# Performance work log

Measured on AMD Instinct MI355X. Metric: run time of the kernel, lower is better.

The kernel has to match this reference:

```python
import math
import jax, jax.numpy as jnp
import numpy as np

NUM_FREQ = 10  # NeRF-style L=10 -> enc dim 3 + 3*2*10 = 63

def pos_encode(coords):
    # freq_bands = 2^i * pi, i = 0..L-1
    freq = (2.0 ** jnp.arange(NUM_FREQ, dtype=coords.dtype)) * math.pi
    scaled = coords[..., None] * freq                      # [E, 3, L]
    enc = jnp.stack([jnp.sin(scaled), jnp.cos(scaled)], axis=-1)  # [E, 3, L, 2]
    enc = enc.reshape(coords.shape[0], -1)                 # [E, 60] interleaved sin/cos
    return jnp.concatenate([coords, enc], axis=-1)         # [E, 63]

def setup_inputs() -> dict:
    key = jax.random.key(0)
    ks = jax.random.split(key, 9)
    N, M, K, C = 65536, 16384, 32, 64
    E = M * K
    x = jax.random.normal(ks[0], (N, C), jnp.float32)
    pos = jax.random.normal(ks[1], (N, 3), jnp.float32)
    batch = jnp.sort(jax.random.randint(ks[2], (N,), 0, 8))
    idx = jax.random.randint(ks[3], (M,), 0, N)
    row = jnp.sort(jax.random.randint(ks[4], (E,), 0, M))
    col = jax.random.randint(ks[5], (E,), 0, N)
    d_in = C + 3 + 3 * 2 * NUM_FREQ  # 127
    def lin(k, i, o):
        s = 1.0 / np.sqrt(i)
        kw, kb = jax.random.split(k)
        return (jax.random.uniform(kw, (i, o), jnp.float32, -s, s),
                jax.random.uniform(kb, (o,), jnp.float32, -s, s))
    lw1, lb1 = lin(ks[6], d_in, 128)
    lw2, lb2 = lin(ks[7], 128, 128)
    gw, gb = lin(ks[8], 128, 256)
    return dict(x=x, pos=pos, batch=batch, idx=idx, row=row, col=col,
                lw1=lw1, lb1=lb1, lw2=lw2, lb2=lb2, gw=gw, gb=gb)

def reference(x, pos, batch, idx, row, col, lw1, lb1, lw2, lb2, gw, gb):
    M = idx.shape[0]
    pos_idx = pos[idx]                         # [M, 3] sampled centers
    pos_diff = pos[col] - pos_idx[row]         # [E, 3] neighbor offsets
    pe = pos_encode(pos_diff)                  # [E, 63]
    edge_in = jnp.concatenate([x[col], pe], axis=-1)   # [E, 127]
    # local_nn: Linear->ReLU->Linear (no final activation, per MLP_Wrapper)
    h = jax.nn.relu(edge_in @ lw1 + lb1)       # [E, 128]
    edge_feat = h @ lw2 + lb2                  # [E, 128]
    # scatter_reduce amax, include_self=False: empty rows stay 0
    agg = jax.ops.segment_max(edge_feat, row, num_segments=M)
    agg = jnp.where(jnp.isneginf(agg), jnp.zeros((), agg.dtype), agg)
    out = agg @ gw + gb                        # [M, 256] global_nn (single Linear)
    return out, pos_idx, batch[idx]
```

## Files before the change

kernel.cpp:

```cpp
#include <hip/hip_runtime.h>
#include <math.h>

#define NN 65536
#define MM 16384
#define EE 524288
#define CF 64
#define HD 128
#define OD 256
#define RPB 16
#define PITCH 129

typedef __bf16 bf16x8 __attribute__((ext_vector_type(8)));
typedef __bf16 bf16x4 __attribute__((ext_vector_type(4)));
typedef float f32x4 __attribute__((ext_vector_type(4)));

__device__ __forceinline__ unsigned enc_f(float f) {
    unsigned u = __float_as_uint(f);
    return (u & 0x80000000u) ? ~u : (u | 0x80000000u);
}
__device__ __forceinline__ float dec_f(unsigned e) {
    unsigned u = (e & 0x80000000u) ? (e ^ 0x80000000u) : ~e;
    return __uint_as_float(u);
}
#define ENC_NEG_INF 0x007FFFFFu

__device__ __forceinline__ unsigned bf_bits(float f) {
    __bf16 b = (__bf16)f;
    return (unsigned)__builtin_bit_cast(unsigned short, b);
}

#define WS_FRAG_OFF 0
#define WS_ROWPTR_OFF 65536
#define WS_XBF_OFF 131072
#define WS_PD_OFF (131072 + 8388608)

__global__ void k_pre(__bf16* __restrict__ fragbuf, int* __restrict__ rowptr,
                      __bf16* __restrict__ xbf, float4* __restrict__ pdbuf,
                      const float* __restrict__ lw1, const float* __restrict__ lw2,
                      const float* __restrict__ x, const int* __restrict__ row,
                      const int* __restrict__ col,
                      const float* __restrict__ pos, const int* __restrict__ batch,
                      const int* __restrict__ idx, float* __restrict__ out) {
    const int b = blockIdx.x;
    const int t = threadIdx.x;
    if (b == 0) {
        const int lane = t & 63;
        const int wv = t >> 6;
        const int q = lane >> 4;
        const int ln = lane & 15;
        #pragma unroll
        for (int fi = 0; fi < 16; ++fi) {
            const int nt = (fi >> 2) & 1, kk = fi & 3;
            const int n = wv * 32 + nt * 16 + ln;
            bf16x8 f;
            #pragma unroll
            for (int j = 0; j < 8; ++j) {
                const int c = kk * 32 + q * 8 + j;
                const int rk = (c < 67) ? c : c - 1;
                f[j] = (fi < 8) ? (__bf16)((c == 67) ? 0.0f : lw1[rk * HD + n])
                                : (__bf16)lw2[c * HD + n];
            }
            *(bf16x8*)&fragbuf[((size_t)fi * 256 + t) * 8] = f;
        }
    } else if (b <= 65) {
        const int i = (b - 1) * 256 + t;
        if (i <= MM) {
            int lo = 0, hi = EE;
            while (lo < hi) { int mid = (lo + hi) >> 1; if (row[mid] < i) lo = mid + 1; else hi = mid; }
            rowptr[i] = lo;
        }
    } else if (b <= 129) {
        const int m = (b - 66) * 256 + t;
        if (m < MM) {
            const int s = idx[m];
            out[MM * OD + m * 3 + 0] = pos[s * 3 + 0];
            out[MM * OD + m * 3 + 1] = pos[s * 3 + 1];
            out[MM * OD + m * 3 + 2] = pos[s * 3 + 2];
            out[MM * OD + MM * 3 + m] = (float)batch[s];
        }
    } else if (b <= 1153) {
        const size_t base = ((size_t)(b - 130) * 256 + t) * 16;
        const float4* xs = (const float4*)(x + base);
        const float4 a = xs[0], c = xs[1], d = xs[2], e = xs[3];
        bf16x8 o0, o1;
        o0[0] = (__bf16)a.x; o0[1] = (__bf16)a.y; o0[2] = (__bf16)a.z; o0[3] = (__bf16)a.w;
        o0[4] = (__bf16)c.x; o0[5] = (__bf16)c.y; o0[6] = (__bf16)c.z; o0[7] = (__bf16)c.w;
        o1[0] = (__bf16)d.x; o1[1] = (__bf16)d.y; o1[2] = (__bf16)d.z; o1[3] = (__bf16)d.w;
        o1[4] = (__bf16)e.x; o1[5] = (__bf16)e.y; o1[6] = (__bf16)e.z; o1[7] = (__bf16)e.w;
        *(bf16x8*)&xbf[base] = o0;
        *(bf16x8*)&xbf[base + 8] = o1;
    } else {
        const int e = (b - 1154) * 256 + t;
        const int r = row[e];
        const int c = col[e];
        const int s = idx[r];
        float4 pd;
        pd.x = pos[c * 3 + 0] - pos[s * 3 + 0];
        pd.y = pos[c * 3 + 1] - pos[s * 3 + 1];
        pd.z = pos[c * 3 + 2] - pos[s * 3 + 2];
        pd.w = 0.0f;
        pdbuf[e] = pd;
    }
}

__launch_bounds__(256)
__global__ void k_fused(const __bf16* __restrict__ xbf, const float4* __restrict__ pdbuf,
                        const int* __restrict__ row, const int* __restrict__ col,
                        const int* __restrict__ rowptr, const __bf16* __restrict__ fragbuf,
                        const float* __restrict__ lb1, const float* __restrict__ lb2,
                        const float* __restrict__ gw, const float* __restrict__ gb,
                        float* __restrict__ out) {
    __shared__ __align__(16) __bf16 einX[64][64];
    __shared__ __align__(16) __bf16 einP[64][64];
    __shared__ __align__(16) __bf16 hbuf[64][HD];
    __shared__ unsigned maxbuf[(RPB + 1) * PITCH];
    __shared__ int srow[2][64];
    const int t = threadIdx.x;
    const int lane = t & 63;
    const int wv = t >> 6;
    const int q = lane >> 4;
    const int ln = lane & 15;
    const int lsw = ln & 7;
    const int m0 = blockIdx.x * RPB;

    const int es = rowptr[m0];
    const int ee = rowptr[m0 + RPB];
    const int ntiles = (ee - es + 63) >> 6;

    for (int i = t; i < (RPB + 1) * PITCH; i += 256) maxbuf[i] = ENC_NEG_INF;

    const int pe_e = t >> 2, pe_part = t & 3, pe_esw = pe_e & 7;
    bf16x8 s0, s1;
    auto issue = [&](int tt) {
        const int eg = min(es + tt * 64 + pe_e, EE - 1);
        const int c = col[eg];
        const bf16x8* xr = (const bf16x8*)(xbf + (size_t)c * CF) + pe_part * 2;
        s0 = xr[0]; s1 = xr[1];
    };
    auto commit = [&]() {
        *(bf16x8*)&einX[pe_e][((pe_part * 2 + 0) ^ pe_esw) * 8] = s0;
        *(bf16x8*)&einX[pe_e][((pe_part * 2 + 1) ^ pe_esw) * 8] = s1;
    };
    auto do_pe = [&](int tt) {
        if (t < 192) {
            const int e = t & 63, d = t >> 6;
            const int sb = tt & 1;
            const int eidx = es + tt * 64 + e;
            const int eg = min(eidx, EE - 1);
            const int esw = e & 7;
            const float4 P = pdbuf[eg];
            const float pd = (d == 0) ? P.x : ((d == 1) ? P.y : P.z);
            if (d == 0) {
                srow[sb][e] = (eidx < ee) ? (row[eg] - m0) : RPB;
                uint2 pkt;
                pkt.x = bf_bits(P.x) | (bf_bits(P.y) << 16);
                pkt.y = bf_bits(P.z);
                *(uint2*)&einP[e][esw * 8] = pkt;
            }
            const float fr = __builtin_amdgcn_fractf(pd * 0.5f);
            float sv = __builtin_amdgcn_sinf(fr);
            float cv = __builtin_amdgcn_cosf(fr);
            #pragma unroll
            for (int l = 0; l < 10; ++l) {
                const int jP = 4 + d * 20 + l * 2;
                *(unsigned*)&einP[e][((jP >> 3) ^ esw) * 8 + (jP & 7)] =
                    bf_bits(sv) | (bf_bits(cv) << 16);
                const float s2 = 2.0f * sv * cv;
                const float c2 = 1.0f - 2.0f * sv * sv;
                sv = s2; cv = c2;
            }
        }
    };

    bf16x8 w1f[2][4];
    #pragma unroll
    for (int nt = 0; nt < 2; ++nt)
        #pragma unroll
        for (int kk = 0; kk < 4; ++kk)
            w1f[nt][kk] = *(const bf16x8*)&fragbuf[((size_t)(nt * 4 + kk) * 256 + t) * 8];
    float4 b1q[2];
    #pragma unroll
    for (int nt = 0; nt < 2; ++nt)
        b1q[nt] = *(const float4*)&lb1[wv * 32 + nt * 16 + q * 4];

    if (ntiles > 0) {
        issue(0);
        commit();
        do_pe(0);
        if (ntiles > 1) issue(1);
    }
    __syncthreads();

    for (int tt = 0; tt < ntiles; ++tt) {
        f32x4 acc[2][4];
        #pragma unroll
        for (int nt = 0; nt < 2; ++nt)
            #pragma unroll
            for (int et = 0; et < 4; ++et)
                acc[nt][et] = (f32x4){b1q[nt].x, b1q[nt].y, b1q[nt].z, b1q[nt].w};
        #pragma unroll
        for (int et = 0; et < 4; ++et) {
            const int e = et * 16 + ln;
            bf16x8 a[4];
            a[0] = *(const bf16x8*)&einX[e][(q ^ lsw) * 8];
            a[1] = *(const bf16x8*)&einX[e][((4 + q) ^ lsw) * 8];
            a[2] = *(const bf16x8*)&einP[e][(q ^ lsw) * 8];
            a[3] = *(const bf16x8*)&einP[e][((4 + q) ^ lsw) * 8];
            #pragma unroll
            for (int kk = 0; kk < 4; ++kk) {
                acc[0][et] = __builtin_amdgcn_mfma_f32_16x16x32_bf16(w1f[0][kk], a[kk], acc[0][et], 0, 0, 0);
                acc[1][et] = __builtin_amdgcn_mfma_f32_16x16x32_bf16(w1f[1][kk], a[kk], acc[1][et], 0, 0, 0);
            }
        }
        #pragma unroll
        for (int et = 0; et < 4; ++et) {
            const int e = et * 16 + ln;
            #pragma unroll
            for (int nt = 0; nt < 2; ++nt) {
                bf16x4 hv;
                hv[0] = (__bf16)fmaxf(acc[nt][et][0], 0.0f);
                hv[1] = (__bf16)fmaxf(acc[nt][et][1], 0.0f);
                hv[2] = (__bf16)fmaxf(acc[nt][et][2], 0.0f);
                hv[3] = (__bf16)fmaxf(acc[nt][et][3], 0.0f);
                const int chunk = wv * 4 + nt * 2 + (q >> 1);
                *(bf16x4*)&hbuf[e][((chunk ^ lsw) * 8) + (q & 1) * 4] = hv;
            }
        }
        __syncthreads();

        {
            if (tt + 1 < ntiles) { commit(); issue(tt + 2 < ntiles ? tt + 2 : tt + 1); }
            bf16x8 w2f[2][4];
            #pragma unroll
            for (int nt = 0; nt < 2; ++nt)
                #pragma unroll
                for (int kk = 0; kk < 4; ++kk)
                    w2f[nt][kk] = *(const bf16x8*)&fragbuf[((size_t)(8 + nt * 4 + kk) * 256 + t) * 8];

            f32x4 acc2[4][2];
            #pragma unroll
            for (int nt = 0; nt < 2; ++nt) {
                const float b2 = lb2[wv * 32 + nt * 16 + ln];
                #pragma unroll
                for (int et = 0; et < 4; ++et)
                    acc2[et][nt] = (f32x4){b2, b2, b2, b2};
            }
            #pragma unroll
            for (int et = 0; et < 4; ++et) {
                const int e = et * 16 + ln;
                #pragma unroll
                for (int kk = 0; kk < 4; ++kk) {
                    bf16x8 ah = *(const bf16x8*)&hbuf[e][((kk * 4 + q) ^ lsw) * 8];
                    acc2[et][0] = __builtin_amdgcn_mfma_f32_16x16x32_bf16(ah, w2f[0][kk], acc2[et][0], 0, 0, 0);
                    acc2[et][1] = __builtin_amdgcn_mfma_f32_16x16x32_bf16(ah, w2f[1][kk], acc2[et][1], 0, 0, 0);
                }
            }
            if (tt + 1 < ntiles) do_pe(tt + 1);
            const int sb = tt & 1;
            #pragma unroll
            for (int et = 0; et < 4; ++et) {
                const int4 R = *(const int4*)&srow[sb][et * 16 + q * 4];
                #pragma unroll
                for (int nt = 0; nt < 2; ++nt) {
                    unsigned* base = maxbuf + (wv * 32 + nt * 16 + ln);
                    const f32x4 vv = acc2[et][nt];
                    int cur = R.x;
                    float m = vv[0];
                    if (R.y != cur) { atomicMax(base + cur * PITCH, enc_f(m)); cur = R.y; m = vv[1]; }
                    else m = fmaxf(m, vv[1]);
                    if (R.z != cur) { atomicMax(base + cur * PITCH, enc_f(m)); cur = R.z; m = vv[2]; }
                    else m = fmaxf(m, vv[2]);
                    if (R.w != cur) { atomicMax(base + cur * PITCH, enc_f(m)); cur = R.w; m = vv[3]; }
                    else m = fmaxf(m, vv[3]);
                    atomicMax(base + cur * PITCH, enc_f(m));
                }
            }
        }
        __syncthreads();
    }

    float* afin = (float*)hbuf;
    for (int i = t; i < RPB * HD; i += 256) {
        const unsigned e = maxbuf[(i >> 7) * PITCH + (i & 127)];
        afin[i] = (e == ENC_NEG_INF) ? 0.0f : dec_f(e);
    }
    __syncthreads();

    const int j4 = (t & 63) * 4;
    const int rbase = (t >> 6) * 4;
    float facc[4][4];
    const float4 bias = *(const float4*)&gb[j4];
    #pragma unroll
    for (int r = 0; r < 4; ++r) { facc[r][0] = bias.x; facc[r][1] = bias.y; facc[r][2] = bias.z; facc[r][3] = bias.w; }
    for (int k = 0; k < 128; k += 4) {
        float4 w0 = *(const float4*)&gw[(k + 0) * OD + j4];
        float4 w1 = *(const float4*)&gw[(k + 1) * OD + j4];
        float4 w2 = *(const float4*)&gw[(k + 2) * OD + j4];
        float4 w3 = *(const float4*)&gw[(k + 3) * OD + j4];
        #pragma unroll
        for (int r = 0; r < 4; ++r) {
            float4 av = *(const float4*)&afin[(rbase + r) * HD + k];
            facc[r][0] += av.x * w0.x + av.y * w1.x + av.z * w2.x + av.w * w3.x;
            facc[r][1] += av.x * w0.y + av.y * w1.y + av.z * w2.y + av.w * w3.y;
            facc[r][2] += av.x * w0.z + av.y * w1.z + av.z * w2.z + av.w * w3.z;
            facc[r][3] += av.x * w0.w + av.y * w1.w + av.z * w2.w + av.w * w3.w;
        }
    }
    #pragma unroll
    for (int r = 0; r < 4; ++r) {
        float4 v; v.x = facc[r][0]; v.y = facc[r][1]; v.z = facc[r][2]; v.w = facc[r][3];
        *(float4*)&out[(size_t)(m0 + rbase + r) * OD + j4] = v;
    }
}

extern "C" void kernel_launch(void* const* d_in, const int* in_sizes, int n_in,
                              void* d_out, int out_size, void* d_ws, size_t ws_size,
                              hipStream_t stream) {
    const float* x   = (const float*)d_in[0];
    const float* pos = (const float*)d_in[1];
    const int* batch = (const int*)d_in[2];
    const int* idx   = (const int*)d_in[3];
    const int* row   = (const int*)d_in[4];
    const int* col   = (const int*)d_in[5];
    const float* lw1 = (const float*)d_in[6];
    const float* lb1 = (const float*)d_in[7];
    const float* lw2 = (const float*)d_in[8];
    const float* lb2 = (const float*)d_in[9];
    const float* gw  = (const float*)d_in[10];
    const float* gb  = (const float*)d_in[11];
    float* out = (float*)d_out;
    __bf16* fragbuf = (__bf16*)((char*)d_ws + WS_FRAG_OFF);
    int* rowptr     = (int*)((char*)d_ws + WS_ROWPTR_OFF);
    __bf16* xbf     = (__bf16*)((char*)d_ws + WS_XBF_OFF);
    float4* pdbuf   = (float4*)((char*)d_ws + WS_PD_OFF);

    hipLaunchKernelGGL(k_pre, dim3(1 + 65 + 64 + 1024 + 2048), dim3(256), 0, stream,
                       fragbuf, rowptr, xbf, pdbuf, lw1, lw2, x, row, col, pos, batch, idx, out);
    hipLaunchKernelGGL(k_fused, dim3(MM / RPB), dim3(256), 0, stream,
                       xbf, pdbuf, row, col, rowptr, fragbuf, lb1, lb2, gw, gb, out);
}
```

Measured before the change: 99.77 us.

## Use 512-thread blocks with each wave owning one 16-column MFMA tile

Doubles the fused kernel's block size to 8 waves so each wave computes a single 16-wide output column slice of both MLP layers instead of two. The weight fragment layout, the gather of x rows (one 16-byte load per thread), the max-scatter and the final global linear are all re-partitioned across 512 threads. This lowers per-thread register pressure and raises the number of waves available to hide gather latency, at the cost of more threads contending for the same barriers and LDS atomics.

```diff
diff --git a/kernel.cpp b/kernel.cpp
--- a/kernel.cpp
+++ b/kernel.cpp
@@ -9,6 +9,7 @@
 #define OD 256
 #define RPB 16
 #define PITCH 129
+#define BT 512
 
 typedef __bf16 bf16x8 __attribute__((ext_vector_type(8)));
 typedef __bf16 bf16x4 __attribute__((ext_vector_type(4)));
@@ -44,23 +45,24 @@
     const int b = blockIdx.x;
     const int t = threadIdx.x;
     if (b == 0) {
-        const int lane = t & 63;
-        const int wv = t >> 6;
-        const int q = lane >> 4;
-        const int ln = lane & 15;
-        #pragma unroll
-        for (int fi = 0; fi < 16; ++fi) {
-            const int nt = (fi >> 2) & 1, kk = fi & 3;
-            const int n = wv * 32 + nt * 16 + ln;
-            bf16x8 f;
-            #pragma unroll
-            for (int j = 0; j < 8; ++j) {
-                const int c = kk * 32 + q * 8 + j;
-                const int rk = (c < 67) ? c : c - 1;
-                f[j] = (fi < 8) ? (__bf16)((c == 67) ? 0.0f : lw1[rk * HD + n])
-                                : (__bf16)lw2[c * HD + n];
-            }
-            *(bf16x8*)&fragbuf[((size_t)fi * 256 + t) * 8] = f;
+        for (int tt = t; tt < BT; tt += 256) {
+            const int lane = tt & 63;
+            const int q = (lane >> 4);
+            const int ln = lane & 15;
+            const int n = (tt >> 6) * 16 + ln;
+            #pragma unroll
+            for (int fi = 0; fi < 8; ++fi) {
+                const int kk = fi & 3;
+                bf16x8 f;
+                #pragma unroll
+                for (int j = 0; j < 8; ++j) {
+                    const int c = kk * 32 + q * 8 + j;
+                    const int rk = (c < 67) ? c : c - 1;
+                    f[j] = (fi < 4) ? (__bf16)((c == 67) ? 0.0f : lw1[rk * HD + n])
+                                    : (__bf16)lw2[c * HD + n];
+                }
+                *(bf16x8*)&fragbuf[((size_t)fi * BT + tt) * 8] = f;
+            }
         }
     } else if (b <= 65) {
         const int i = (b - 1) * 256 + t;
@@ -103,7 +105,7 @@
     }
 }
 
-__launch_bounds__(256)
+__launch_bounds__(BT)
 __global__ void k_fused(const __bf16* __restrict__ xbf, const float4* __restrict__ pdbuf,
                         const int* __restrict__ row, const int* __restrict__ col,
                         const int* __restrict__ rowptr, const __bf16* __restrict__ fragbuf,
@@ -121,25 +123,24 @@
     const int q = lane >> 4;
     const int ln = lane & 15;
     const int lsw = ln & 7;
+    const int n0 = wv * 16;
     const int m0 = blockIdx.x * RPB;
 
     const int es = rowptr[m0];
     const int ee = rowptr[m0 + RPB];
     const int ntiles = (ee - es + 63) >> 6;
 
-    for (int i = t; i < (RPB + 1) * PITCH; i += 256) maxbuf[i] = ENC_NEG_INF;
-
-    const int pe_e = t >> 2, pe_part = t & 3, pe_esw = pe_e & 7;
-    bf16x8 s0, s1;
+    for (int i = t; i < (RPB + 1) * PITCH; i += BT) maxbuf[i] = ENC_NEG_INF;
+
+    const int pe_e = t >> 3, pe_part = t & 7, pe_esw = pe_e & 7;
+    bf16x8 s0;
     auto issue = [&](int tt) {
         const int eg = min(es + tt * 64 + pe_e, EE - 1);
         const int c = col[eg];
-        const bf16x8* xr = (const bf16x8*)(xbf + (size_t)c * CF) + pe_part * 2;
-        s0 = xr[0]; s1 = xr[1];
+        s0 = *(const bf16x8*)(xbf + (size_t)c * CF + pe_part * 8);
     };
     auto commit = [&]() {
-        *(bf16x8*)&einX[pe_e][((pe_part * 2 + 0) ^ pe_esw) * 8] = s0;
-        *(bf16x8*)&einX[pe_e][((pe_part * 2 + 1) ^ pe_esw) * 8] = s1;
+        *(bf16x8*)&einX[pe_e][(pe_part ^ pe_esw) * 8] = s0;
     };
     auto do_pe = [&](int tt) {
         if (t < 192) {
@@ -172,16 +173,11 @@
         }
     };
 
-    bf16x8 w1f[2][4];
+    bf16x8 w1f[4];
     #pragma unroll
-    for (int nt = 0; nt < 2; ++nt)
-        #pragma unroll
-        for (int kk = 0; kk < 4; ++kk)
-            w1f[nt][kk] = *(const bf16x8*)&fragbuf[((size_t)(nt * 4 + kk) * 256 + t) * 8];
-    float4 b1q[2];
-    #pragma unroll
-    for (int nt = 0; nt < 2; ++nt)
-        b1q[nt] = *(const float4*)&lb1[wv * 32 + nt * 16 + q * 4];
+    for (int kk = 0; kk < 4; ++kk)
+        w1f[kk] = *(const bf16x8*)&fragbuf[((size_t)kk * BT + t) * 8];
+    const float4 b1q = *(const float4*)&lb1[n0 + q * 4];
 
     if (ntiles > 0) {
         issue(0);
@@ -192,12 +188,10 @@
     __syncthreads();
 
     for (int tt = 0; tt < ntiles; ++tt) {
-        f32x4 acc[2][4];
+        f32x4 acc[4];
         #pragma unroll
-        for (int nt = 0; nt < 2; ++nt)
-            #pragma unroll
-            for (int et = 0; et < 4; ++et)
-                acc[nt][et] = (f32x4){b1q[nt].x, b1q[nt].y, b1q[nt].z, b1q[nt].w};
+        for (int et = 0; et < 4; ++et)
+            acc[et] = (f32x4){b1q.x, b1q.y, b1q.z, b1q.w};
         #pragma unroll
         for (int et = 0; et < 4; ++et) {
             const int e = et * 16 + ln;
@@ -207,52 +201,41 @@
             a[2] = *(const bf16x8*)&einP[e][(q ^ lsw) * 8];
             a[3] = *(const bf16x8*)&einP[e][((4 + q) ^ lsw) * 8];
             #pragma unroll
-            for (int kk = 0; kk < 4; ++kk) {
-                acc[0][et] = __builtin_amdgcn_mfma_f32_16x16x32_bf16(w1f[0][kk], a[kk], acc[0][et], 0, 0, 0);
-                acc[1][et] = __builtin_amdgcn_mfma_f32_16x16x32_bf16(w1f[1][kk], a[kk], acc[1][et], 0, 0, 0);
-            }
+            for (int kk = 0; kk < 4; ++kk)
+                acc[et] = __builtin_amdgcn_mfma_f32_16x16x32_bf16(w1f[kk], a[kk], acc[et], 0, 0, 0);
         }
         #pragma unroll
         for (int et = 0; et < 4; ++et) {
             const int e = et * 16 + ln;
-            #pragma unroll
-            for (int nt = 0; nt < 2; ++nt) {
-                bf16x4 hv;
-                hv[0] = (__bf16)fmaxf(acc[nt][et][0], 0.0f);
-                hv[1] = (__bf16)fmaxf(acc[nt][et][1], 0.0f);
-                hv[2] = (__bf16)fmaxf(acc[nt][et][2], 0.0f);
-                hv[3] = (__bf16)fmaxf(acc[nt][et][3], 0.0f);
-                const int chunk = wv * 4 + nt * 2 + (q >> 1);
-                *(bf16x4*)&hbuf[e][((chunk ^ lsw) * 8) + (q & 1) * 4] = hv;
-            }
+            bf16x4 hv;
+            hv[0] = (__bf16)fmaxf(acc[et][0], 0.0f);
+            hv[1] = (__bf16)fmaxf(acc[et][1], 0.0f);
+            hv[2] = (__bf16)fmaxf(acc[et][2], 0.0f);
+            hv[3] = (__bf16)fmaxf(acc[et][3], 0.0f);
+            const int chunk = wv * 2 + (q >> 1);
+            *(bf16x4*)&hbuf[e][((chunk ^ lsw) * 8) + (q & 1) * 4] = hv;
         }
         __syncthreads();
 
         {
             if (tt + 1 < ntiles) { commit(); issue(tt + 2 < ntiles ? tt + 2 : tt + 1); }
-            bf16x8 w2f[2][4];
-            #pragma unroll
-            for (int nt = 0; nt < 2; ++nt)
-                #pragma unroll
-                for (int kk = 0; kk < 4; ++kk)
-                    w2f[nt][kk] = *(const bf16x8*)&fragbuf[((size_t)(8 + nt * 4 + kk) * 256 + t) * 8];
-
-            f32x4 acc2[4][2];
-            #pragma unroll
-            for (int nt = 0; nt < 2; ++nt) {
-                const float b2 = lb2[wv * 32 + nt * 16 + ln];
-                #pragma unroll
-                for (int et = 0; et < 4; ++et)
-                    acc2[et][nt] = (f32x4){b2, b2, b2, b2};
-            }
+            bf16x8 w2f[4];
+            #pragma unroll
+            for (int kk = 0; kk < 4; ++kk)
+                w2f[kk] = *(const bf16x8*)&fragbuf[((size_t)(4 + kk) * BT + t) * 8];
+
+            const float b2 = lb2[n0 + ln];
+            f32x4 acc2[4];
+            #pragma unroll
+            for (int et = 0; et < 4; ++et)
+                acc2[et] = (f32x4){b2, b2, b2, b2};
             #pragma unroll
             for (int et = 0; et < 4; ++et) {
                 const int e = et * 16 + ln;
                 #pragma unroll
                 for (int kk = 0; kk < 4; ++kk) {
                     bf16x8 ah = *(const bf16x8*)&hbuf[e][((kk * 4 + q) ^ lsw) * 8];
-                    acc2[et][0] = __builtin_amdgcn_mfma_f32_16x16x32_bf16(ah, w2f[0][kk], acc2[et][0], 0, 0, 0);
-                    acc2[et][1] = __builtin_amdgcn_mfma_f32_16x16x32_bf16(ah, w2f[1][kk], acc2[et][1], 0, 0, 0);
+                    acc2[et] = __builtin_amdgcn_mfma_f32_16x16x32_bf16(ah, w2f[kk], acc2[et], 0, 0, 0);
                 }
             }
             if (tt + 1 < ntiles) do_pe(tt + 1);
@@ -260,45 +243,42 @@
             #pragma unroll
             for (int et = 0; et < 4; ++et) {
                 const int4 R = *(const int4*)&srow[sb][et * 16 + q * 4];
-                #pragma unroll
-                for (int nt = 0; nt < 2; ++nt) {
-                    unsigned* base = maxbuf + (wv * 32 + nt * 16 + ln);
-                    const f32x4 vv = acc2[et][nt];
-                    int cur = R.x;
-                    float m = vv[0];
-                    if (R.y != cur) { atomicMax(base + cur * PITCH, enc_f(m)); cur = R.y; m = vv[1]; }
-                    else m = fmaxf(m, vv[1]);
-                    if (R.z != cur) { atomicMax(base + cur * PITCH, enc_f(m)); cur = R.z; m = vv[2]; }
-                    else m = fmaxf(m, vv[2]);
-                    if (R.w != cur) { atomicMax(base + cur * PITCH, enc_f(m)); cur = R.w; m = vv[3]; }
-                    else m = fmaxf(m, vv[3]);
-                    atomicMax(base + cur * PITCH, enc_f(m));
-                }
+                unsigned* base = maxbuf + (n0 + ln);
+                const f32x4 vv = acc2[et];
+                int cur = R.x;
+                float m = vv[0];
+                if (R.y != cur) { atomicMax(base + cur * PITCH, enc_f(m)); cur = R.y; m = vv[1]; }
+                else m = fmaxf(m, vv[1]);
+                if (R.z != cur) { atomicMax(base + cur * PITCH, enc_f(m)); cur = R.z; m = vv[2]; }
+                else m = fmaxf(m, vv[2]);
+                if (R.w != cur) { atomicMax(base + cur * PITCH, enc_f(m)); cur = R.w; m = vv[3]; }
+                else m = fmaxf(m, vv[3]);
+                atomicMax(base + cur * PITCH, enc_f(m));
             }
         }
         __syncthreads();
     }
 
     float* afin = (float*)hbuf;
-    for (int i = t; i < RPB * HD; i += 256) {
+    for (int i = t; i < RPB * HD; i += BT) {
         const unsigned e = maxbuf[(i >> 7) * PITCH + (i & 127)];
         afin[i] = (e == ENC_NEG_INF) ? 0.0f : dec_f(e);
     }
     __syncthreads();
 
     const int j4 = (t & 63) * 4;
-    const int rbase = (t >> 6) * 4;
-    float facc[4][4];
+    const int rbase = (t >> 6) * 2;
+    float facc[2][4];
     const float4 bias = *(const float4*)&gb[j4];
     #pragma unroll
-    for (int r = 0; r < 4; ++r) { facc[r][0] = bias.x; facc[r][1] = bias.y; facc[r][2] = bias.z; facc[r][3] = bias.w; }
+    for (int r = 0; r < 2; ++r) { facc[r][0] = bias.x; facc[r][1] = bias.y; facc[r][2] = bias.z; facc[r][3] = bias.w; }
     for (int k = 0; k < 128; k += 4) {
         float4 w0 = *(const float4*)&gw[(k + 0) * OD + j4];
         float4 w1 = *(const float4*)&gw[(k + 1) * OD + j4];
         float4 w2 = *(const float4*)&gw[(k + 2) * OD + j4];
         float4 w3 = *(const float4*)&gw[(k + 3) * OD + j4];
         #pragma unroll
-        for (int r = 0; r < 4; ++r) {
+        for (int r = 0; r < 2; ++r) {
             float4 av = *(const float4*)&afin[(rbase + r) * HD + k];
             facc[r][0] += av.x * w0.x + av.y * w1.x + av.z * w2.x + av.w * w3.x;
             facc[r][1] += av.x * w0.y + av.y * w1.y + av.z * w2.y + av.w * w3.y;
@@ -307,7 +287,7 @@
         }
     }
     #pragma unroll
-    for (int r = 0; r < 4; ++r) {
+    for (int r = 0; r < 2; ++r) {
         float4 v; v.x = facc[r][0]; v.y = facc[r][1]; v.z = facc[r][2]; v.w = facc[r][3];
         *(float4*)&out[(size_t)(m0 + rbase + r) * OD + j4] = v;
     }
@@ -336,6 +316,6 @@
 
     hipLaunchKernelGGL(k_pre, dim3(1 + 65 + 64 + 1024 + 2048), dim3(256), 0, stream,
                        fragbuf, rowptr, xbf, pdbuf, lw1, lw2, x, row, col, pos, batch, idx, out);
-    hipLaunchKernelGGL(k_fused, dim3(MM / RPB), dim3(256), 0, stream,
+    hipLaunchKernelGGL(k_fused, dim3(MM / RPB), dim3(BT), 0, stream,
                        xbf, pdbuf, row, col, rowptr, fragbuf, lb1, lb2, gw, gb, out);
 }
```

After: 104.4 us. 4.7% more time.

## Load gathered x rows directly into MFMA fragments, dropping LDS staging

Applied to the files above, without the earlier changes.

Removes the einX shared-memory buffer and the software-pipelined issue/commit prefetch of gathered x[col] rows. Each wave now loads its col indices and reads its bf16 x fragments straight from global memory into registers just before the first-layer MFMAs. This saves LDS space and LDS write/read traffic, which may help occupancy. The cost is that the gather latency is no longer hidden behind the previous tile's work, and the four waves each fetch the same rows redundantly.

```diff
diff --git a/kernel.cpp b/kernel.cpp
--- a/kernel.cpp
+++ b/kernel.cpp
@@ -110,7 +110,6 @@
                         const float* __restrict__ lb1, const float* __restrict__ lb2,
                         const float* __restrict__ gw, const float* __restrict__ gb,
                         float* __restrict__ out) {
-    __shared__ __align__(16) __bf16 einX[64][64];
     __shared__ __align__(16) __bf16 einP[64][64];
     __shared__ __align__(16) __bf16 hbuf[64][HD];
     __shared__ unsigned maxbuf[(RPB + 1) * PITCH];
@@ -129,18 +128,6 @@
 
     for (int i = t; i < (RPB + 1) * PITCH; i += 256) maxbuf[i] = ENC_NEG_INF;
 
-    const int pe_e = t >> 2, pe_part = t & 3, pe_esw = pe_e & 7;
-    bf16x8 s0, s1;
-    auto issue = [&](int tt) {
-        const int eg = min(es + tt * 64 + pe_e, EE - 1);
-        const int c = col[eg];
-        const bf16x8* xr = (const bf16x8*)(xbf + (size_t)c * CF) + pe_part * 2;
-        s0 = xr[0]; s1 = xr[1];
-    };
-    auto commit = [&]() {
-        *(bf16x8*)&einX[pe_e][((pe_part * 2 + 0) ^ pe_esw) * 8] = s0;
-        *(bf16x8*)&einX[pe_e][((pe_part * 2 + 1) ^ pe_esw) * 8] = s1;
-    };
     auto do_pe = [&](int tt) {
         if (t < 192) {
             const int e = t & 63, d = t >> 6;
@@ -183,15 +170,17 @@
     for (int nt = 0; nt < 2; ++nt)
         b1q[nt] = *(const float4*)&lb1[wv * 32 + nt * 16 + q * 4];
 
-    if (ntiles > 0) {
-        issue(0);
-        commit();
-        do_pe(0);
-        if (ntiles > 1) issue(1);
-    }
+    if (ntiles > 0) do_pe(0);
     __syncthreads();
 
     for (int tt = 0; tt < ntiles; ++tt) {
+        const int ebase = es + tt * 64;
+
+        int cvals[4];
+        #pragma unroll
+        for (int et = 0; et < 4; ++et)
+            cvals[et] = col[min(ebase + et * 16 + ln, EE - 1)];
+
         f32x4 acc[2][4];
         #pragma unroll
         for (int nt = 0; nt < 2; ++nt)
@@ -201,16 +190,19 @@
         #pragma unroll
         for (int et = 0; et < 4; ++et) {
             const int e = et * 16 + ln;
-            bf16x8 a[4];
-            a[0] = *(const bf16x8*)&einX[e][(q ^ lsw) * 8];
-            a[1] = *(const bf16x8*)&einX[e][((4 + q) ^ lsw) * 8];
-            a[2] = *(const bf16x8*)&einP[e][(q ^ lsw) * 8];
-            a[3] = *(const bf16x8*)&einP[e][((4 + q) ^ lsw) * 8];
-            #pragma unroll
-            for (int kk = 0; kk < 4; ++kk) {
-                acc[0][et] = __builtin_amdgcn_mfma_f32_16x16x32_bf16(w1f[0][kk], a[kk], acc[0][et], 0, 0, 0);
-                acc[1][et] = __builtin_amdgcn_mfma_f32_16x16x32_bf16(w1f[1][kk], a[kk], acc[1][et], 0, 0, 0);
-            }
+            const __bf16* xp = xbf + (size_t)cvals[et] * CF + q * 8;
+            bf16x8 a0 = *(const bf16x8*)xp;
+            bf16x8 a1 = *(const bf16x8*)(xp + 32);
+            bf16x8 a2 = *(const bf16x8*)&einP[e][(q ^ lsw) * 8];
+            bf16x8 a3 = *(const bf16x8*)&einP[e][((4 + q) ^ lsw) * 8];
+            acc[0][et] = __builtin_amdgcn_mfma_f32_16x16x32_bf16(w1f[0][0], a0, acc[0][et], 0, 0, 0);
+            acc[1][et] = __builtin_amdgcn_mfma_f32_16x16x32_bf16(w1f[1][0], a0, acc[1][et], 0, 0, 0);
+            acc[0][et] = __builtin_amdgcn_mfma_f32_16x16x32_bf16(w1f[0][1], a1, acc[0][et], 0, 0, 0);
+            acc[1][et] = __builtin_amdgcn_mfma_f32_16x16x32_bf16(w1f[1][1], a1, acc[1][et], 0, 0, 0);
+            acc[0][et] = __builtin_amdgcn_mfma_f32_16x16x32_bf16(w1f[0][2], a2, acc[0][et], 0, 0, 0);
+            acc[1][et] = __builtin_amdgcn_mfma_f32_16x16x32_bf16(w1f[1][2], a2, acc[1][et], 0, 0, 0);
+            acc[0][et] = __builtin_amdgcn_mfma_f32_16x16x32_bf16(w1f[0][3], a3, acc[0][et], 0, 0, 0);
+            acc[1][et] = __builtin_amdgcn_mfma_f32_16x16x32_bf16(w1f[1][3], a3, acc[1][et], 0, 0, 0);
         }
         #pragma unroll
         for (int et = 0; et < 4; ++et) {
@@ -229,7 +221,6 @@
         __syncthreads();
 
         {
-            if (tt + 1 < ntiles) { commit(); issue(tt + 2 < ntiles ? tt + 2 : tt + 1); }
             bf16x8 w2f[2][4];
             #pragma unroll
             for (int nt = 0; nt < 2; ++nt)
```

Result: slower. 121.7 us (+21.9%).

## Enlarge edge tile to 128 and restructure gather prefetch schedule

Applied to the files above, without the earlier changes.

Doubles the per-iteration edge tile from 64 to 128 edges, processing each tile as two 64-edge halves for both MLP layers. The goal is fewer barriers and loop iterations per block and more work between synchronisations. The x-feature gather prefetch now runs one tile ahead and is issued during the first layer-1 half instead of two tiles ahead. Shared memory use roughly doubles, which may lower occupancy, and the shorter prefetch distance could expose more gather latency.

```diff
diff --git a/kernel.cpp b/kernel.cpp
--- a/kernel.cpp
+++ b/kernel.cpp
@@ -8,6 +8,7 @@
 #define HD 128
 #define OD 256
 #define RPB 16
+#define ET 128
 #define PITCH 129
 
 typedef __bf16 bf16x8 __attribute__((ext_vector_type(8)));
@@ -110,11 +111,11 @@
                         const float* __restrict__ lb1, const float* __restrict__ lb2,
                         const float* __restrict__ gw, const float* __restrict__ gb,
                         float* __restrict__ out) {
-    __shared__ __align__(16) __bf16 einX[64][64];
-    __shared__ __align__(16) __bf16 einP[64][64];
-    __shared__ __align__(16) __bf16 hbuf[64][HD];
+    __shared__ __align__(16) __bf16 einX[ET][64];
+    __shared__ __align__(16) __bf16 einP[ET][64];
+    __shared__ __align__(16) __bf16 hbuf[ET][HD];
     __shared__ unsigned maxbuf[(RPB + 1) * PITCH];
-    __shared__ int srow[2][64];
+    __shared__ int srow[2][ET];
     const int t = threadIdx.x;
     const int lane = t & 63;
     const int wv = t >> 6;
@@ -125,49 +126,55 @@
 
     const int es = rowptr[m0];
     const int ee = rowptr[m0 + RPB];
-    const int ntiles = (ee - es + 63) >> 6;
+    const int ntiles = (ee - es + ET - 1) >> 7;
 
     for (int i = t; i < (RPB + 1) * PITCH; i += 256) maxbuf[i] = ENC_NEG_INF;
 
-    const int pe_e = t >> 2, pe_part = t & 3, pe_esw = pe_e & 7;
-    bf16x8 s0, s1;
+    const int pe_e = t >> 1, pe_part = t & 1, pe_esw = pe_e & 7;
+    bf16x8 s0, s1, s2, s3;
     auto issue = [&](int tt) {
-        const int eg = min(es + tt * 64 + pe_e, EE - 1);
+        const int eg = min(es + tt * ET + pe_e, EE - 1);
         const int c = col[eg];
-        const bf16x8* xr = (const bf16x8*)(xbf + (size_t)c * CF) + pe_part * 2;
-        s0 = xr[0]; s1 = xr[1];
+        const bf16x8* xr = (const bf16x8*)(xbf + (size_t)c * CF + pe_part * 32);
+        s0 = xr[0]; s1 = xr[1]; s2 = xr[2]; s3 = xr[3];
     };
     auto commit = [&]() {
-        *(bf16x8*)&einX[pe_e][((pe_part * 2 + 0) ^ pe_esw) * 8] = s0;
-        *(bf16x8*)&einX[pe_e][((pe_part * 2 + 1) ^ pe_esw) * 8] = s1;
+        *(bf16x8*)&einX[pe_e][((pe_part * 4 + 0) ^ pe_esw) * 8] = s0;
+        *(bf16x8*)&einX[pe_e][((pe_part * 4 + 1) ^ pe_esw) * 8] = s1;
+        *(bf16x8*)&einX[pe_e][((pe_part * 4 + 2) ^ pe_esw) * 8] = s2;
+        *(bf16x8*)&einX[pe_e][((pe_part * 4 + 3) ^ pe_esw) * 8] = s3;
     };
     auto do_pe = [&](int tt) {
-        if (t < 192) {
-            const int e = t & 63, d = t >> 6;
-            const int sb = tt & 1;
-            const int eidx = es + tt * 64 + e;
-            const int eg = min(eidx, EE - 1);
-            const int esw = e & 7;
-            const float4 P = pdbuf[eg];
-            const float pd = (d == 0) ? P.x : ((d == 1) ? P.y : P.z);
-            if (d == 0) {
-                srow[sb][e] = (eidx < ee) ? (row[eg] - m0) : RPB;
-                uint2 pkt;
-                pkt.x = bf_bits(P.x) | (bf_bits(P.y) << 16);
-                pkt.y = bf_bits(P.z);
-                *(uint2*)&einP[e][esw * 8] = pkt;
-            }
-            const float fr = __builtin_amdgcn_fractf(pd * 0.5f);
-            float sv = __builtin_amdgcn_sinf(fr);
-            float cv = __builtin_amdgcn_cosf(fr);
-            #pragma unroll
-            for (int l = 0; l < 10; ++l) {
-                const int jP = 4 + d * 20 + l * 2;
-                *(unsigned*)&einP[e][((jP >> 3) ^ esw) * 8 + (jP & 7)] =
-                    bf_bits(sv) | (bf_bits(cv) << 16);
-                const float s2 = 2.0f * sv * cv;
-                const float c2 = 1.0f - 2.0f * sv * sv;
-                sv = s2; cv = c2;
+        const int sb = tt & 1;
+        #pragma unroll
+        for (int i = 0; i < 2; ++i) {
+            const int p = i * 256 + t;
+            if (p < 384) {
+                const int e = p & 127, d = p >> 7;
+                const int eidx = es + tt * ET + e;
+                const int eg = min(eidx, EE - 1);
+                const int esw = e & 7;
+                const float4 P = pdbuf[eg];
+                const float pd = (d == 0) ? P.x : ((d == 1) ? P.y : P.z);
+                if (d == 0) {
+                    srow[sb][e] = (eidx < ee) ? (row[eg] - m0) : RPB;
+                    uint2 pkt;
+                    pkt.x = bf_bits(P.x) | (bf_bits(P.y) << 16);
+                    pkt.y = bf_bits(P.z);
+                    *(uint2*)&einP[e][esw * 8] = pkt;
+                }
+                const float fr = __builtin_amdgcn_fractf(pd * 0.5f);
+                float sv = __builtin_amdgcn_sinf(fr);
+                float cv = __builtin_amdgcn_cosf(fr);
+                #pragma unroll
+                for (int l = 0; l < 10; ++l) {
+                    const int jP = 4 + d * 20 + l * 2;
+                    *(unsigned*)&einP[e][((jP >> 3) ^ esw) * 8 + (jP & 7)] =
+                        bf_bits(sv) | (bf_bits(cv) << 16);
+                    const float s2 = 2.0f * sv * cv;
+                    const float c2 = 1.0f - 2.0f * sv * sv;
+                    sv = s2; cv = c2;
+                }
             }
         }
     };
@@ -192,88 +199,95 @@
     __syncthreads();
 
     for (int tt = 0; tt < ntiles; ++tt) {
-        f32x4 acc[2][4];
-        #pragma unroll
-        for (int nt = 0; nt < 2; ++nt)
-            #pragma unroll
-            for (int et = 0; et < 4; ++et)
-                acc[nt][et] = (f32x4){b1q[nt].x, b1q[nt].y, b1q[nt].z, b1q[nt].w};
-        #pragma unroll
-        for (int et = 0; et < 4; ++et) {
-            const int e = et * 16 + ln;
-            bf16x8 a[4];
-            a[0] = *(const bf16x8*)&einX[e][(q ^ lsw) * 8];
-            a[1] = *(const bf16x8*)&einX[e][((4 + q) ^ lsw) * 8];
-            a[2] = *(const bf16x8*)&einP[e][(q ^ lsw) * 8];
-            a[3] = *(const bf16x8*)&einP[e][((4 + q) ^ lsw) * 8];
-            #pragma unroll
-            for (int kk = 0; kk < 4; ++kk) {
-                acc[0][et] = __builtin_amdgcn_mfma_f32_16x16x32_bf16(w1f[0][kk], a[kk], acc[0][et], 0, 0, 0);
-                acc[1][et] = __builtin_amdgcn_mfma_f32_16x16x32_bf16(w1f[1][kk], a[kk], acc[1][et], 0, 0, 0);
-            }
-        }
-        #pragma unroll
-        for (int et = 0; et < 4; ++et) {
-            const int e = et * 16 + ln;
-            #pragma unroll
-            for (int nt = 0; nt < 2; ++nt) {
-                bf16x4 hv;
-                hv[0] = (__bf16)fmaxf(acc[nt][et][0], 0.0f);
-                hv[1] = (__bf16)fmaxf(acc[nt][et][1], 0.0f);
-                hv[2] = (__bf16)fmaxf(acc[nt][et][2], 0.0f);
-                hv[3] = (__bf16)fmaxf(acc[nt][et][3], 0.0f);
-                const int chunk = wv * 4 + nt * 2 + (q >> 1);
-                *(bf16x4*)&hbuf[e][((chunk ^ lsw) * 8) + (q & 1) * 4] = hv;
+        #pragma unroll
+        for (int hh = 0; hh < 2; ++hh) {
+            f32x4 acc[2][4];
+            #pragma unroll
+            for (int nt = 0; nt < 2; ++nt)
+                #pragma unroll
+                for (int et = 0; et < 4; ++et)
+                    acc[nt][et] = (f32x4){b1q[nt].x, b1q[nt].y, b1q[nt].z, b1q[nt].w};
+            #pragma unroll
+            for (int et = 0; et < 4; ++et) {
+                const int e = hh * 64 + et * 16 + ln;
+                bf16x8 a[4];
+                a[0] = *(const bf16x8*)&einX[e][(q ^ lsw) * 8];
+                a[1] = *(const bf16x8*)&einX[e][((4 + q) ^ lsw) * 8];
+                a[2] = *(const bf16x8*)&einP[e][(q ^ lsw) * 8];
+                a[3] = *(const bf16x8*)&einP[e][((4 + q) ^ lsw) * 8];
+                #pragma unroll
+                for (int kk = 0; kk < 4; ++kk) {
+                    acc[0][et] = __builtin_amdgcn_mfma_f32_16x16x32_bf16(w1f[0][kk], a[kk], acc[0][et], 0, 0, 0);
+                    acc[1][et] = __builtin_amdgcn_mfma_f32_16x16x32_bf16(w1f[1][kk], a[kk], acc[1][et], 0, 0, 0);
+                }
+            }
+            if (hh == 0 && tt + 1 < ntiles) issue(tt + 1);
+            #pragma unroll
+            for (int et = 0; et < 4; ++et) {
+                const int e = hh * 64 + et * 16 + ln;
+                #pragma unroll
+                for (int nt = 0; nt < 2; ++nt) {
+                    bf16x4 hv;
+                    hv[0] = (__bf16)fmaxf(acc[nt][et][0], 0.0f);
+                    hv[1] = (__bf16)fmaxf(acc[nt][et][1], 0.0f);
+                    hv[2] = (__bf16)fmaxf(acc[nt][et][2], 0.0f);
+                    hv[3] = (__bf16)fmaxf(acc[nt][et][3], 0.0f);
+                    const int chunk = wv * 4 + nt * 2 + (q >> 1);
+                    *(bf16x4*)&hbuf[e][((chunk ^ lsw) * 8) + (q & 1) * 4] = hv;
+                }
             }
         }
         __syncthreads();
 
         {
-            if (tt + 1 < ntiles) { commit(); issue(tt + 2 < ntiles ? tt + 2 : tt + 1); }
+            if (tt + 1 < ntiles) commit();
             bf16x8 w2f[2][4];
             #pragma unroll
             for (int nt = 0; nt < 2; ++nt)
                 #pragma unroll
                 for (int kk = 0; kk < 4; ++kk)
                     w2f[nt][kk] = *(const bf16x8*)&fragbuf[((size_t)(8 + nt * 4 + kk) * 256 + t) * 8];
-
-            f32x4 acc2[4][2];
-            #pragma unroll
-            for (int nt = 0; nt < 2; ++nt) {
-                const float b2 = lb2[wv * 32 + nt * 16 + ln];
-                #pragma unroll
-                for (int et = 0; et < 4; ++et)
-                    acc2[et][nt] = (f32x4){b2, b2, b2, b2};
-            }
-            #pragma unroll
-            for (int et = 0; et < 4; ++et) {
-                const int e = et * 16 + ln;
-                #pragma unroll
-                for (int kk = 0; kk < 4; ++kk) {
-                    bf16x8 ah = *(const bf16x8*)&hbuf[e][((kk * 4 + q) ^ lsw) * 8];
-                    acc2[et][0] = __builtin_amdgcn_mfma_f32_16x16x32_bf16(ah, w2f[0][kk], acc2[et][0], 0, 0, 0);
-                    acc2[et][1] = __builtin_amdgcn_mfma_f32_16x16x32_bf16(ah, w2f[1][kk], acc2[et][1], 0, 0, 0);
-                }
-            }
-            if (tt + 1 < ntiles) do_pe(tt + 1);
             const int sb = tt & 1;
-            #pragma unroll
-            for (int et = 0; et < 4; ++et) {
-                const int4 R = *(const int4*)&srow[sb][et * 16 + q * 4];
+
+            #pragma unroll
+            for (int hh = 0; hh < 2; ++hh) {
+                f32x4 acc2[4][2];
                 #pragma unroll
                 for (int nt = 0; nt < 2; ++nt) {
-                    unsigned* base = maxbuf + (wv * 32 + nt * 16 + ln);
-                    const f32x4 vv = acc2[et][nt];
-                    int cur = R.x;
-                    float m = vv[0];
-                    if (R.y != cur) { atomicMax(base + cur * PITCH, enc_f(m)); cur = R.y; m = vv[1]; }
-                    else m = fmaxf(m, vv[1]);
-                    if (R.z != cur) { atomicMax(base + cur * PITCH, enc_f(m)); cur = R.z; m = vv[2]; }
-                    else m = fmaxf(m, vv[2]);
-                    if (R.w != cur) { atomicMax(base + cur * PITCH, enc_f(m)); cur = R.w; m = vv[3]; }
-                    else m = fmaxf(m, vv[3]);
-                    atomicMax(base + cur * PITCH, enc_f(m));
-                }
+                    const float b2 = lb2[wv * 32 + nt * 16 + ln];
+                    #pragma unroll
+                    for (int et = 0; et < 4; ++et)
+                        acc2[et][nt] = (f32x4){b2, b2, b2, b2};
+                }
+                #pragma unroll
+                for (int et = 0; et < 4; ++et) {
+                    const int e = hh * 64 + et * 16 + ln;
+                    #pragma unroll
+                    for (int kk = 0; kk < 4; ++kk) {
+                        bf16x8 ah = *(const bf16x8*)&hbuf[e][((kk * 4 + q) ^ lsw) * 8];
+                        acc2[et][0] = __builtin_amdgcn_mfma_f32_16x16x32_bf16(ah, w2f[0][kk], acc2[et][0], 0, 0, 0);
+                        acc2[et][1] = __builtin_amdgcn_mfma_f32_16x16x32_bf16(ah, w2f[1][kk], acc2[et][1], 0, 0, 0);
+                    }
+                }
+                #pragma unroll
+                for (int et = 0; et < 4; ++et) {
+                    const int4 R = *(const int4*)&srow[sb][hh * 64 + et * 16 + q * 4];
+                    #pragma unroll
+                    for (int nt = 0; nt < 2; ++nt) {
+                        unsigned* base = maxbuf + (wv * 32 + nt * 16 + ln);
+                        const f32x4 vv = acc2[et][nt];
+                        int cur = R.x;
+                        float m = vv[0];
+                        if (R.y != cur) { atomicMax(base + cur * PITCH, enc_f(m)); cur = R.y; m = vv[1]; }
+                        else m = fmaxf(m, vv[1]);
+                        if (R.z != cur) { atomicMax(base + cur * PITCH, enc_f(m)); cur = R.z; m = vv[2]; }
+                        else m = fmaxf(m, vv[2]);
+                        if (R.w != cur) { atomicMax(base + cur * PITCH, enc_f(m)); cur = R.w; m = vv[3]; }
+                        else m = fmaxf(m, vv[3]);
+                        atomicMax(base + cur * PITCH, enc_f(m));
+                    }
+                }
+                if (hh == 0 && tt + 1 < ntiles) do_pe(tt + 1);
             }
         }
         __syncthreads();
```

Measured after the change: 101.7 us. No clear change (+1.9%).
